# Optimization experiments

Hardware: AMD Instinct MI355X
Metric: run time of the kernel (lower is better)

Reference implementation:

```python
import jax, jax.numpy as jnp
import numpy as np

N = 50000      # nodes
E = 800000     # edges in normalized A (incl. self loops)
DIN = 128      # input_dim
DOUT = 64      # output_dim
BN_EPS = 1e-5
SLOPE = 0.01   # LeakyReLU default negative slope


def setup_inputs() -> dict:
    key = jax.random.key(0)
    ks = jax.random.split(key, 10)
    H = jax.random.normal(ks[0], (N, DIN), dtype=jnp.float32)
    rows = jax.random.randint(ks[1], (E,), 0, N, dtype=jnp.int32)
    cols = jax.random.randint(ks[2], (E,), 0, N, dtype=jnp.int32)
    # values of the symmetrically normalized adjacency (precomputed in __init__)
    vals = jax.random.uniform(ks[3], (E,), dtype=jnp.float32)
    # BatchNorm1d params/buffers (eval mode: use running stats)
    gamma = 1.0 + 0.1 * jax.random.normal(ks[4], (DIN,), dtype=jnp.float32)
    beta = 0.1 * jax.random.normal(ks[5], (DIN,), dtype=jnp.float32)
    run_mean = 0.1 * jax.random.normal(ks[6], (DIN,), dtype=jnp.float32)
    run_var = 0.5 + jax.random.uniform(ks[7], (DIN,), dtype=jnp.float32)
    # Linear(input_dim, output_dim)
    W = jax.random.normal(ks[8], (DIN, DOUT), dtype=jnp.float32) / np.sqrt(DIN)
    b = 0.01 * jax.random.normal(ks[9], (DOUT,), dtype=jnp.float32)
    return dict(H=H, rows=rows, cols=cols, vals=vals, gamma=gamma, beta=beta,
                run_mean=run_mean, run_var=run_var, W=W, b=b)


def reference(H, rows, cols, vals, gamma, beta, run_mean, run_var, W, b):
    # F.normalize: L2 row normalization with eps=1e-12
    norm = jnp.maximum(jnp.linalg.norm(H, axis=1, keepdims=True), 1e-12)
    Hn = H / norm
    # BatchNorm1d (eval: running stats); dropout is identity in eval
    scale = gamma * jax.lax.rsqrt(run_var + BN_EPS)
    Hb = (Hn - run_mean) * scale + beta
    # Linear projection [N, DIN] @ [DIN, DOUT]
    X = Hb @ W + b
    # SpMM: out[r] = sum_{e: rows[e]==r} vals[e] * X[cols[e]]
    msgs = vals[:, None] * X[cols]            # [E, DOUT] gather + scale
    out = jax.ops.segment_sum(msgs, rows, num_segments=N)
    # LeakyReLU
    return jnp.where(out >= 0, out, SLOPE * out)
```

## Files before the change

### kernel.cpp

```cpp
#include <hip/hip_runtime.h>
#include <hip/hip_fp16.h>

#define N_NODES 50000
#define E_EDGES 800000
#define DIN 128
#define DOUT 64
#define NBUK 196
#define BUKCAP 4608
#define CHUNK 2048
#define NBLKA 391
#define ASTRIDE 136

typedef short short8 __attribute__((ext_vector_type(8)));
typedef float f32x4 __attribute__((ext_vector_type(4)));

static __device__ __forceinline__ short f2bf(float f)
{
    union { float f; unsigned u; } x{f};
    const unsigned r = x.u + 0x7FFFu + ((x.u >> 16) & 1u);
    return (short)(r >> 16);
}

__global__ __launch_bounds__(256) void k_x(
    const float* __restrict__ H, const float* __restrict__ gamma,
    const float* __restrict__ beta, const float* __restrict__ mean,
    const float* __restrict__ var, const float* __restrict__ W,
    const float* __restrict__ bias, unsigned short* __restrict__ X16,
    int* __restrict__ gcursor)
{
    __shared__ short A_s[64][ASTRIDE];
    __shared__ short B_s[64][ASTRIDE];
    const int t = threadIdx.x;
    const int l = t & 63, wv = t >> 6;
    const int R0 = blockIdx.x * 64;

    if (blockIdx.x == 0 && t < NBUK) gcursor[t] = 0;

    {
        const int n = t >> 2, koff = (t & 3) * 32;
#pragma unroll
        for (int i = 0; i < 16; ++i) {
            const int k = koff + i * 2;
            const unsigned lo = (unsigned short)f2bf(W[k * DOUT + n]);
            const unsigned hi = (unsigned short)f2bf(W[(k + 1) * DOUT + n]);
            *(unsigned*)&B_s[n][k] = lo | (hi << 16);
        }
    }
    {
        const int rloc = t >> 2, sub = t & 3;
        const int r = R0 + rloc;
        float4 h[8];
        if (r < N_NODES) {
            const float4* hp = (const float4*)(H + (size_t)r * DIN + sub * 32);
#pragma unroll
            for (int i = 0; i < 8; ++i) h[i] = hp[i];
        } else {
#pragma unroll
            for (int i = 0; i < 8; ++i) h[i] = make_float4(0.f, 0.f, 0.f, 0.f);
        }
        float ss = 0.f;
#pragma unroll
        for (int i = 0; i < 8; ++i)
            ss += h[i].x * h[i].x + h[i].y * h[i].y + h[i].z * h[i].z + h[i].w * h[i].w;
        ss += __shfl_xor(ss, 1, 64);
        ss += __shfl_xor(ss, 2, 64);
        const float inv = 1.0f / fmaxf(sqrtf(ss), 1e-12f);

        const float4* gp = (const float4*)(gamma + sub * 32);
        const float4* bp = (const float4*)(beta  + sub * 32);
        const float4* mp = (const float4*)(mean  + sub * 32);
        const float4* vp = (const float4*)(var   + sub * 32);
#pragma unroll
        for (int i = 0; i < 8; ++i) {
            const float4 g4 = gp[i], b4 = bp[i], m4 = mp[i], v4 = vp[i];
            const float s0 = g4.x * rsqrtf(v4.x + 1e-5f);
            const float s1 = g4.y * rsqrtf(v4.y + 1e-5f);
            const float s2 = g4.z * rsqrtf(v4.z + 1e-5f);
            const float s3 = g4.w * rsqrtf(v4.w + 1e-5f);
            const float e0 = h[i].x * inv * s0 + (b4.x - m4.x * s0);
            const float e1 = h[i].y * inv * s1 + (b4.y - m4.y * s1);
            const float e2 = h[i].z * inv * s2 + (b4.z - m4.z * s2);
            const float e3 = h[i].w * inv * s3 + (b4.w - m4.w * s3);
            const unsigned u0 = (unsigned short)f2bf(e0) | ((unsigned)(unsigned short)f2bf(e1) << 16);
            const unsigned u1 = (unsigned short)f2bf(e2) | ((unsigned)(unsigned short)f2bf(e3) << 16);
            *(uint2*)&A_s[rloc][sub * 32 + i * 4] = make_uint2(u0, u1);
        }
    }

    const int ml = l & 15, q = l >> 4;
    f32x4 c0, c1, c2, c3;
    {
        const float b0 = bias[ml],      b1 = bias[16 + ml];
        const float b2 = bias[32 + ml], b3 = bias[48 + ml];
        c0 = f32x4{b0, b0, b0, b0};
        c1 = f32x4{b1, b1, b1, b1};
        c2 = f32x4{b2, b2, b2, b2};
        c3 = f32x4{b3, b3, b3, b3};
    }
    __syncthreads();

#pragma unroll
    for (int k0 = 0; k0 < 4; ++k0) {
        const short8 a  = *(const short8*)&A_s[wv * 16 + ml][k0 * 32 + q * 8];
        const short8 b0 = *(const short8*)&B_s[ml][k0 * 32 + q * 8];
        const short8 b1 = *(const short8*)&B_s[16 + ml][k0 * 32 + q * 8];
        const short8 b2 = *(const short8*)&B_s[32 + ml][k0 * 32 + q * 8];
        const short8 b3 = *(const short8*)&B_s[48 + ml][k0 * 32 + q * 8];
        c0 = __builtin_amdgcn_mfma_f32_16x16x32_bf16(a, b0, c0, 0, 0, 0);
        c1 = __builtin_amdgcn_mfma_f32_16x16x32_bf16(a, b1, c1, 0, 0, 0);
        c2 = __builtin_amdgcn_mfma_f32_16x16x32_bf16(a, b2, c2, 0, 0, 0);
        c3 = __builtin_amdgcn_mfma_f32_16x16x32_bf16(a, b3, c3, 0, 0, 0);
    }

    __syncthreads();
    unsigned short* otile = (unsigned short*)&A_s[0][0];
#pragma unroll
    for (int i = 0; i < 4; ++i) {
        const int r = wv * 16 + q * 4 + i;
        otile[r * 64 + ml]      = __half_as_ushort(__float2half(c0[i]));
        otile[r * 64 + 16 + ml] = __half_as_ushort(__float2half(c1[i]));
        otile[r * 64 + 32 + ml] = __half_as_ushort(__float2half(c2[i]));
        otile[r * 64 + 48 + ml] = __half_as_ushort(__float2half(c3[i]));
    }
    __syncthreads();
#pragma unroll
    for (int rep = 0; rep < 2; ++rep) {
        const int id = rep * 256 + t;
        const int row = id >> 3;
        const int off = (id & 7) * 8;
        if (R0 + row < N_NODES)
            *(uint4*)(X16 + (size_t)(R0 + row) * DOUT + off) =
                *(const uint4*)&otile[row * 64 + off];
    }
}

__global__ __launch_bounds__(512) void k_passA(
    const int* __restrict__ rows, const int* __restrict__ cols,
    const float* __restrict__ vals, int* __restrict__ gcursor,
    unsigned* __restrict__ midVC, unsigned char* __restrict__ midR)
{
    __shared__ int lhist[NBUK], lstart[NBUK], lcur[NBUK], gbase[NBUK];
    __shared__ int scn[256];
    __shared__ unsigned lbinVC[CHUNK];
    __shared__ unsigned short lbinBR[CHUNK];
    const int t = threadIdx.x;
    const int e0 = blockIdx.x * CHUNK;
    const int nC = min(CHUNK, E_EDGES - e0);

    if (t < NBUK) lhist[t] = 0;
    __syncthreads();

    unsigned prVC[4];
    unsigned short prBR[4];
#pragma unroll
    for (int k = 0; k < 4; ++k) {
        const int e = e0 + k * 512 + t;
        if (e < E_EDGES) {
            const int r = rows[e];
            const unsigned hv = __half_as_ushort(__float2half(vals[e]));
            prVC[k] = (hv << 16) | (unsigned)cols[e];
            prBR[k] = (unsigned short)r;
            atomicAdd(&lhist[r >> 8], 1);
        } else {
            prBR[k] = 0xFFFFu;
        }
    }
    __syncthreads();

    const int v = (t < NBUK) ? lhist[t] : 0;
    if (t < 256) scn[t] = v;
    __syncthreads();
    for (int o = 1; o < 256; o <<= 1) {
        int u = 0;
        if (t < 256 && t >= o) u = scn[t - o];
        __syncthreads();
        if (t < 256) scn[t] += u;
        __syncthreads();
    }
    if (t < NBUK) {
        const int ex = scn[t] - v;
        lstart[t] = ex;
        lcur[t] = ex;
        gbase[t] = t * BUKCAP + (v ? atomicAdd(&gcursor[t], v) : 0);
    }
    __syncthreads();

#pragma unroll
    for (int k = 0; k < 4; ++k) {
        if (prBR[k] != 0xFFFFu) {
            const int bk = prBR[k] >> 8;
            const int pos = atomicAdd(&lcur[bk], 1);
            lbinVC[pos] = prVC[k];
            lbinBR[pos] = prBR[k];
        }
    }
    __syncthreads();

    for (int i = t; i < nC; i += 512) {
        const unsigned short br = lbinBR[i];
        const int bk = br >> 8;
        const int g = gbase[bk] + (i - lstart[bk]);
        if (g < (bk + 1) * BUKCAP) {
            midVC[g] = lbinVC[i];
            midR[g] = (unsigned char)(br & 255);
        }
    }
}

__global__ __launch_bounds__(512) void k_passB(
    const int* __restrict__ gcursor, const unsigned* __restrict__ midVC,
    const unsigned char* __restrict__ midR, unsigned* __restrict__ ev,
    int* __restrict__ rowS, int* __restrict__ rowE)
{
    __shared__ int lhist[256], scn[256], lcur[256];
    const int t = threadIdx.x;
    const int b = blockIdx.x;
    const int base = b * BUKCAP;
    const int total = min(gcursor[b], BUKCAP);

    if (t < 256) lhist[t] = 0;
    __syncthreads();
    for (int i = t; i < total; i += 512)
        atomicAdd(&lhist[midR[base + i]], 1);
    __syncthreads();

    const int v = (t < 256) ? lhist[t] : 0;
    if (t < 256) scn[t] = v;
    __syncthreads();
    for (int o = 1; o < 256; o <<= 1) {
        int u = 0;
        if (t < 256 && t >= o) u = scn[t - o];
        __syncthreads();
        if (t < 256) scn[t] += u;
        __syncthreads();
    }
    if (t < 256) {
        const int ex = scn[t] - v;
        lcur[t] = ex;
        const int gr = (b << 8) | t;
        if (gr < N_NODES) { rowS[gr] = base + ex; rowE[gr] = base + ex + v; }
    }
    __syncthreads();

    for (int i = t; i < total; i += 512) {
        const int lr = midR[base + i];
        const int pos = atomicAdd(&lcur[lr], 1);
        ev[base + pos] = midVC[base + i];
    }
}

__global__ __launch_bounds__(256) void k_spmm(
    const int* __restrict__ rowS, const int* __restrict__ rowE,
    const unsigned* __restrict__ ev, const unsigned short* __restrict__ X16,
    float* __restrict__ out)
{
    const int lane = threadIdx.x & 63;
    const int hl   = lane & 31;
    const int h    = lane >> 5;
    const int row  = blockIdx.x * 4 + (threadIdx.x >> 6);
    const int s  = rowS[row];
    const int e2 = rowE[row];
    float ax = 0.f, ay = 0.f;
    for (int c = s; c < e2; c += 64) {
        const int idx = c + lane;
        unsigned p = 0;
        if (idx < e2) p = ev[idx];
        const int cnt  = min(e2 - c, 64);
        const int jmax = (cnt + 1) >> 1;
        int j = 0;
        for (; j + 1 < jmax; j += 2) {
            const unsigned u0 = (unsigned)__shfl((int)p, 2 * j + h,     64);
            const unsigned u1 = (unsigned)__shfl((int)p, 2 * j + 2 + h, 64);
            const unsigned x0 = *(const unsigned*)(X16 + (u0 & 0xFFFFu) * DOUT + 2 * hl);
            const unsigned x1 = *(const unsigned*)(X16 + (u1 & 0xFFFFu) * DOUT + 2 * hl);
            const float v0 = __half2float(__ushort_as_half((unsigned short)(u0 >> 16)));
            const float v1 = __half2float(__ushort_as_half((unsigned short)(u1 >> 16)));
            const float2 f0 = __half22float2(*(const __half2*)&x0);
            const float2 f1 = __half22float2(*(const __half2*)&x1);
            ax = fmaf(v0, f0.x, ax); ay = fmaf(v0, f0.y, ay);
            ax = fmaf(v1, f1.x, ax); ay = fmaf(v1, f1.y, ay);
        }
        for (; j < jmax; ++j) {
            const unsigned u = (unsigned)__shfl((int)p, 2 * j + h, 64);
            const unsigned x = *(const unsigned*)(X16 + (u & 0xFFFFu) * DOUT + 2 * hl);
            const float v = __half2float(__ushort_as_half((unsigned short)(u >> 16)));
            const float2 f = __half22float2(*(const __half2*)&x);
            ax = fmaf(v, f.x, ax); ay = fmaf(v, f.y, ay);
        }
    }
    ax += __shfl_xor(ax, 32, 64);
    ay += __shfl_xor(ay, 32, 64);
    if (h == 0) {
        float2 r;
        r.x = (ax >= 0.f) ? ax : 0.01f * ax;
        r.y = (ay >= 0.f) ? ay : 0.01f * ay;
        *(float2*)(out + (size_t)row * DOUT + 2 * hl) = r;
    }
}

extern "C" void kernel_launch(void* const* d_in, const int* in_sizes, int n_in,
                              void* d_out, int out_size, void* d_ws, size_t ws_size,
                              hipStream_t stream)
{
    const float* H     = (const float*)d_in[0];
    const int*   rows  = (const int*)  d_in[1];
    const int*   cols  = (const int*)  d_in[2];
    const float* vals  = (const float*)d_in[3];
    const float* gamma = (const float*)d_in[4];
    const float* beta  = (const float*)d_in[5];
    const float* mean  = (const float*)d_in[6];
    const float* var   = (const float*)d_in[7];
    const float* W     = (const float*)d_in[8];
    const float* bias  = (const float*)d_in[9];
    float* out = (float*)d_out;

    char* ws = (char*)d_ws;
    unsigned short* X16     = (unsigned short*)(ws);
    int*            gcursor = (int*)          (ws +  6400000);
    unsigned*       midVC   = (unsigned*)     (ws +  6400800);
    unsigned char*  midR    = (unsigned char*)(ws + 10013472);
    unsigned*       ev      = (unsigned*)     (ws + 10916640);
    int*            rowS    = (int*)          (ws + 14529312);
    int*            rowE    = (int*)          (ws + 14730016);

    k_x<<<(N_NODES + 63) / 64, 256, 0, stream>>>(H, gamma, beta, mean, var, W,
                                                 bias, X16, gcursor);
    k_passA<<<NBLKA, 512, 0, stream>>>(rows, cols, vals, gcursor, midVC, midR);
    k_passB<<<NBUK, 512, 0, stream>>>(gcursor, midVC, midR, ev, rowS, rowE);
    k_spmm<<<N_NODES / 4, 256, 0, stream>>>(rowS, rowE, ev, X16, out);
}
```

Before: 157.1 us.

## Split bucket sort into 32-row groups, use wave scans, widen SpMM gathers

Pass B now runs 8 blocks per 256-row bucket. Each block handles a 32-row group with its own fixed-capacity output region, which gives far more blocks than the 196 used before. Both pass A and pass B replace the multi-barrier LDS prefix scans with wavefront shuffle scans. The SpMM has each lane gather 8 bytes (4 fp16 values) so a wave processes 4 edges at once, and row start/end are packed into an int2. In exchange, each block in pass B rescans the whole bucket, which means 8x redundant reads of midR, and edges are silently dropped if a 32-row group exceeds its per-group capacity.

```diff
diff --git a/kernel.cpp b/kernel.cpp
--- a/kernel.cpp
+++ b/kernel.cpp
@@ -9,6 +9,8 @@
 #define BUKCAP 4608
 #define CHUNK 2048
 #define NBLKA 391
+#define NGRP 1563
+#define GCAP 704
 #define ASTRIDE 136
 
 typedef short short8 __attribute__((ext_vector_type(8)));
@@ -140,10 +142,11 @@
     unsigned* __restrict__ midVC, unsigned char* __restrict__ midR)
 {
     __shared__ int lhist[NBUK], lstart[NBUK], lcur[NBUK], gbase[NBUK];
-    __shared__ int scn[256];
+    __shared__ int wsumS[4];
     __shared__ unsigned lbinVC[CHUNK];
     __shared__ unsigned short lbinBR[CHUNK];
     const int t = threadIdx.x;
+    const int lane = t & 63, wv = t >> 6;
     const int e0 = blockIdx.x * CHUNK;
     const int nC = min(CHUNK, E_EDGES - e0);
 
@@ -168,17 +171,20 @@
     __syncthreads();
 
     const int v = (t < NBUK) ? lhist[t] : 0;
-    if (t < 256) scn[t] = v;
-    __syncthreads();
-    for (int o = 1; o < 256; o <<= 1) {
-        int u = 0;
-        if (t < 256 && t >= o) u = scn[t - o];
-        __syncthreads();
-        if (t < 256) scn[t] += u;
-        __syncthreads();
-    }
+    int x = v;
+    if (t < 256) {
+#pragma unroll
+        for (int o = 1; o < 64; o <<= 1) {
+            const int y = __shfl_up(x, o, 64);
+            if (lane >= o) x += y;
+        }
+        if (lane == 63) wsumS[wv] = x;
+    }
+    __syncthreads();
     if (t < NBUK) {
-        const int ex = scn[t] - v;
+        int pre = 0;
+        for (int i = 0; i < wv; ++i) pre += wsumS[i];
+        const int ex = pre + x - v;
         lstart[t] = ex;
         lcur[t] = ex;
         gbase[t] = t * BUKCAP + (v ? atomicAdd(&gcursor[t], v) : 0);
@@ -207,94 +213,106 @@
     }
 }
 
-__global__ __launch_bounds__(512) void k_passB(
+__global__ __launch_bounds__(256) void k_passB(
     const int* __restrict__ gcursor, const unsigned* __restrict__ midVC,
     const unsigned char* __restrict__ midR, unsigned* __restrict__ ev,
-    int* __restrict__ rowS, int* __restrict__ rowE)
-{
-    __shared__ int lhist[256], scn[256], lcur[256];
+    int2* __restrict__ rowSE)
+{
+    __shared__ int lhist[32], lcur[32];
+    const int g  = blockIdx.x;
+    const int bk = g >> 3;
+    const int q  = g & 7;
+    const int base = bk * BUKCAP;
+    const int total = min(gcursor[bk], BUKCAP);
     const int t = threadIdx.x;
-    const int b = blockIdx.x;
-    const int base = b * BUKCAP;
-    const int total = min(gcursor[b], BUKCAP);
-
-    if (t < 256) lhist[t] = 0;
-    __syncthreads();
-    for (int i = t; i < total; i += 512)
-        atomicAdd(&lhist[midR[base + i]], 1);
-    __syncthreads();
-
-    const int v = (t < 256) ? lhist[t] : 0;
-    if (t < 256) scn[t] = v;
-    __syncthreads();
-    for (int o = 1; o < 256; o <<= 1) {
-        int u = 0;
-        if (t < 256 && t >= o) u = scn[t - o];
-        __syncthreads();
-        if (t < 256) scn[t] += u;
-        __syncthreads();
-    }
-    if (t < 256) {
-        const int ex = scn[t] - v;
-        lcur[t] = ex;
-        const int gr = (b << 8) | t;
-        if (gr < N_NODES) { rowS[gr] = base + ex; rowE[gr] = base + ex + v; }
-    }
-    __syncthreads();
-
-    for (int i = t; i < total; i += 512) {
+
+    if (t < 32) lhist[t] = 0;
+    __syncthreads();
+    for (int i = t; i < total; i += 256) {
         const int lr = midR[base + i];
-        const int pos = atomicAdd(&lcur[lr], 1);
-        ev[base + pos] = midVC[base + i];
+        if ((lr >> 5) == q) atomicAdd(&lhist[lr & 31], 1);
+    }
+    __syncthreads();
+    if (t < 32) {
+        const int v = lhist[t];
+        int x = v;
+#pragma unroll
+        for (int o = 1; o < 32; o <<= 1) {
+            const int y = __shfl_up(x, o, 64);
+            if (t >= o) x += y;
+        }
+        const int ex = x - v;
+        lcur[t] = min(ex, GCAP);
+        const int row = (g << 5) | t;
+        if (row < N_NODES)
+            rowSE[row] = make_int2(g * GCAP + min(ex, GCAP),
+                                   g * GCAP + min(ex + v, GCAP));
+    }
+    __syncthreads();
+    for (int i = t; i < total; i += 256) {
+        const int lr = midR[base + i];
+        if ((lr >> 5) == q) {
+            const int pos = atomicAdd(&lcur[lr & 31], 1);
+            if (pos < GCAP) ev[g * GCAP + pos] = midVC[base + i];
+        }
     }
 }
 
 __global__ __launch_bounds__(256) void k_spmm(
-    const int* __restrict__ rowS, const int* __restrict__ rowE,
-    const unsigned* __restrict__ ev, const unsigned short* __restrict__ X16,
-    float* __restrict__ out)
+    const int2* __restrict__ rowSE, const unsigned* __restrict__ ev,
+    const unsigned short* __restrict__ X16, float* __restrict__ out)
 {
     const int lane = threadIdx.x & 63;
-    const int hl   = lane & 31;
-    const int h    = lane >> 5;
+    const int ql   = lane & 15;
+    const int qh   = lane >> 4;
     const int row  = blockIdx.x * 4 + (threadIdx.x >> 6);
-    const int s  = rowS[row];
-    const int e2 = rowE[row];
-    float ax = 0.f, ay = 0.f;
+    const int2 se = rowSE[row];
+    const int s = se.x, e2 = se.y;
+    float a0 = 0.f, a1 = 0.f, a2 = 0.f, a3 = 0.f;
     for (int c = s; c < e2; c += 64) {
         const int idx = c + lane;
         unsigned p = 0;
         if (idx < e2) p = ev[idx];
         const int cnt  = min(e2 - c, 64);
-        const int jmax = (cnt + 1) >> 1;
+        const int jmax = (cnt + 3) >> 2;
         int j = 0;
         for (; j + 1 < jmax; j += 2) {
-            const unsigned u0 = (unsigned)__shfl((int)p, 2 * j + h,     64);
-            const unsigned u1 = (unsigned)__shfl((int)p, 2 * j + 2 + h, 64);
-            const unsigned x0 = *(const unsigned*)(X16 + (u0 & 0xFFFFu) * DOUT + 2 * hl);
-            const unsigned x1 = *(const unsigned*)(X16 + (u1 & 0xFFFFu) * DOUT + 2 * hl);
+            const unsigned u0 = (unsigned)__shfl((int)p, 4 * j + qh,     64);
+            const unsigned u1 = (unsigned)__shfl((int)p, 4 * j + 4 + qh, 64);
+            const uint2 x0 = *(const uint2*)(X16 + (u0 & 0xFFFFu) * DOUT + 4 * ql);
+            const uint2 x1 = *(const uint2*)(X16 + (u1 & 0xFFFFu) * DOUT + 4 * ql);
             const float v0 = __half2float(__ushort_as_half((unsigned short)(u0 >> 16)));
             const float v1 = __half2float(__ushort_as_half((unsigned short)(u1 >> 16)));
-            const float2 f0 = __half22float2(*(const __half2*)&x0);
-            const float2 f1 = __half22float2(*(const __half2*)&x1);
-            ax = fmaf(v0, f0.x, ax); ay = fmaf(v0, f0.y, ay);
-            ax = fmaf(v1, f1.x, ax); ay = fmaf(v1, f1.y, ay);
+            const float2 f00 = __half22float2(*(const __half2*)&x0.x);
+            const float2 f01 = __half22float2(*(const __half2*)&x0.y);
+            const float2 f10 = __half22float2(*(const __half2*)&x1.x);
+            const float2 f11 = __half22float2(*(const __half2*)&x1.y);
+            a0 = fmaf(v0, f00.x, a0); a1 = fmaf(v0, f00.y, a1);
+            a2 = fmaf(v0, f01.x, a2); a3 = fmaf(v0, f01.y, a3);
+            a0 = fmaf(v1, f10.x, a0); a1 = fmaf(v1, f10.y, a1);
+            a2 = fmaf(v1, f11.x, a2); a3 = fmaf(v1, f11.y, a3);
         }
         for (; j < jmax; ++j) {
-            const unsigned u = (unsigned)__shfl((int)p, 2 * j + h, 64);
-            const unsigned x = *(const unsigned*)(X16 + (u & 0xFFFFu) * DOUT + 2 * hl);
+            const unsigned u = (unsigned)__shfl((int)p, 4 * j + qh, 64);
+            const uint2 xx = *(const uint2*)(X16 + (u & 0xFFFFu) * DOUT + 4 * ql);
             const float v = __half2float(__ushort_as_half((unsigned short)(u >> 16)));
-            const float2 f = __half22float2(*(const __half2*)&x);
-            ax = fmaf(v, f.x, ax); ay = fmaf(v, f.y, ay);
-        }
-    }
-    ax += __shfl_xor(ax, 32, 64);
-    ay += __shfl_xor(ay, 32, 64);
-    if (h == 0) {
-        float2 r;
-        r.x = (ax >= 0.f) ? ax : 0.01f * ax;
-        r.y = (ay >= 0.f) ? ay : 0.01f * ay;
-        *(float2*)(out + (size_t)row * DOUT + 2 * hl) = r;
+            const float2 f0 = __half22float2(*(const __half2*)&xx.x);
+            const float2 f1 = __half22float2(*(const __half2*)&xx.y);
+            a0 = fmaf(v, f0.x, a0); a1 = fmaf(v, f0.y, a1);
+            a2 = fmaf(v, f1.x, a2); a3 = fmaf(v, f1.y, a3);
+        }
+    }
+    a0 += __shfl_xor(a0, 16, 64); a0 += __shfl_xor(a0, 32, 64);
+    a1 += __shfl_xor(a1, 16, 64); a1 += __shfl_xor(a1, 32, 64);
+    a2 += __shfl_xor(a2, 16, 64); a2 += __shfl_xor(a2, 32, 64);
+    a3 += __shfl_xor(a3, 16, 64); a3 += __shfl_xor(a3, 32, 64);
+    if (lane < 16) {
+        float4 r;
+        r.x = (a0 >= 0.f) ? a0 : 0.01f * a0;
+        r.y = (a1 >= 0.f) ? a1 : 0.01f * a1;
+        r.z = (a2 >= 0.f) ? a2 : 0.01f * a2;
+        r.w = (a3 >= 0.f) ? a3 : 0.01f * a3;
+        *(float4*)(out + (size_t)row * DOUT + 4 * ql) = r;
     }
 }
 
@@ -320,12 +338,11 @@
     unsigned*       midVC   = (unsigned*)     (ws +  6400800);
     unsigned char*  midR    = (unsigned char*)(ws + 10013472);
     unsigned*       ev      = (unsigned*)     (ws + 10916640);
-    int*            rowS    = (int*)          (ws + 14529312);
-    int*            rowE    = (int*)          (ws + 14730016);
+    int2*           rowSE   = (int2*)         (ws + 15318048);
 
     k_x<<<(N_NODES + 63) / 64, 256, 0, stream>>>(H, gamma, beta, mean, var, W,
                                                  bias, X16, gcursor);
     k_passA<<<NBLKA, 512, 0, stream>>>(rows, cols, vals, gcursor, midVC, midR);
-    k_passB<<<NBUK, 512, 0, stream>>>(gcursor, midVC, midR, ev, rowS, rowE);
-    k_spmm<<<N_NODES / 4, 256, 0, stream>>>(rowS, rowE, ev, X16, out);
-}
+    k_passB<<<NGRP, 256, 0, stream>>>(gcursor, midVC, midR, ev, rowSE);
+    k_spmm<<<N_NODES / 4, 256, 0, stream>>>(rowSE, ev, X16, out);
+}
```

Measured after the change: 160.6 us. 2.2% more time.
